# Kernel optimization log

Measured on AMD Instinct MI355X. Metric: run time of the kernel, lower is better.

Reference implementation:

```python
import jax, jax.numpy as jnp
import numpy as np

SCALE_DIM = 64  # output_size, used as 1/sqrt(d) scale per source code


def setup_inputs() -> dict:
    key = jax.random.key(0)
    ks = jax.random.split(key, 6)
    B, S, D_IN, D_OUT = 4, 4096, 512, 64
    return {
        "key_inputs": jax.random.normal(ks[0], (B, S, D_IN), dtype=jnp.float32),
        "value_inputs": jax.random.normal(ks[1], (B, S, D_IN), dtype=jnp.float32),
        "query_inputs": jax.random.normal(ks[2], (B, S, D_IN), dtype=jnp.float32),
        "Wq": jax.random.normal(ks[3], (D_IN, D_OUT), dtype=jnp.float32) * 0.05,
        "Wk": jax.random.normal(ks[4], (D_IN, D_OUT), dtype=jnp.float32) * 0.05,
        "Wv": jax.random.normal(ks[5], (D_IN, D_OUT), dtype=jnp.float32) * 0.05,
    }


def reference(key_inputs, value_inputs, query_inputs, Wq, Wk, Wv):
    # QKV projections: [B,S,D_in] x [D_in,D_out] -> [B,S,D_out]
    Q = jnp.einsum("bsd,de->bse", query_inputs, Wq)
    K = jnp.einsum("bsd,de->bse", key_inputs, Wk)
    V = jnp.einsum("bsd,de->bse", value_inputs, Wv)
    d = K.shape[2]
    # scores: [B, Sq, Sk]
    scores = jnp.einsum("bqe,bke->bqk", Q, K) / jnp.sqrt(jnp.float32(d))
    # causal mask: strictly-upper-triangular -inf (source: transpose(tril(-inf, -1)))
    Sq, Sk = Q.shape[1], K.shape[1]
    causal = jnp.tril(jnp.ones((Sq, Sk), dtype=bool))
    scores = jnp.where(causal[None, :, :], scores, -jnp.inf)
    attn = jax.nn.softmax(scores, axis=-1)
    Z = jnp.einsum("bqk,bke->bqe", attn, V)
    return Z
```

## Files before the change

kernel.cpp:

```cpp
#include <hip/hip_runtime.h>
#include <hip/hip_bf16.h>

#define BATCH 4
#define SEQ   4096
#define DIN   512
#define DOUT  64

typedef __attribute__((ext_vector_type(4))) float f32x4;
typedef __attribute__((ext_vector_type(8))) short bf16x8;
typedef __attribute__((ext_vector_type(4))) short bf16x4;

__device__ __forceinline__ f32x4 mfma16(bf16x8 a, bf16x8 b, f32x4 c) {
    return __builtin_amdgcn_mfma_f32_16x16x32_bf16(a, b, c, 0, 0, 0);
}
__device__ __forceinline__ f32x4 mfma16k(bf16x4 a, bf16x4 b, f32x4 c) {
    return __builtin_amdgcn_mfma_f32_16x16x16bf16_1k(a, b, c, 0, 0, 0);
}

__device__ __forceinline__ short f2bf(float f) {
    union { float f; unsigned u; } x; x.f = f;
    unsigned r = x.u + 0x7FFFu + ((x.u >> 16) & 1u);
    return (short)(r >> 16);
}

__device__ __forceinline__ unsigned pack_bf2(float lo, float hi) {
    union { float f; unsigned u; } a, b; a.f = lo; b.f = hi;
    return __builtin_amdgcn_perm(b.u, a.u, 0x07060302u);
}

__device__ __forceinline__ void dma16(const void* g, void* l) {
    __builtin_amdgcn_global_load_lds(
        (const __attribute__((address_space(1))) void*)g,
        (__attribute__((address_space(3))) void*)l, 16, 0, 0);
}

#define QSCALE 0.1803368801111204f

__global__ __launch_bounds__(256) void wconv_kernel(
    const float* __restrict__ Wq, const float* __restrict__ Wk,
    const float* __restrict__ Wv, short* __restrict__ Wt)
{
    const int m = blockIdx.y;
    const float* W = (m == 0) ? Wq : (m == 1) ? Wk : Wv;
    const int idx = blockIdx.x * 256 + threadIdx.x;
    const int k = idx >> 6;
    const int n = idx & 63;
    Wt[m * (DOUT * DIN) + n * DIN + k] = f2bf(W[idx]);
}

__global__ __launch_bounds__(256) void proj_kernel(
    const float* __restrict__ Xq, const float* __restrict__ Xk, const float* __restrict__ Xv,
    const short* __restrict__ Wt,
    short* __restrict__ Qb, short* __restrict__ Kb, short* __restrict__ Vt)
{
    __shared__ __align__(16) char smem[2][24576];

    const int m = blockIdx.y;
    const float* X  = (m == 0) ? Xq : (m == 1) ? Xk : Xv;
    const short* Wm = Wt + m * (DOUT * DIN);

    const int tid  = threadIdx.x;
    const int wv   = tid >> 6;
    const int lane = tid & 63;
    const int quad = lane >> 4;
    const int l16  = lane & 15;
    const long waveRow = (long)blockIdx.x * 64 + wv * 16;

    const float* xg = X  + (waveRow + l16) * DIN + quad * 8;
    const short* wg = Wm + (long)(wv * 16 + l16) * DIN + quad * 8;

    f32x4 acc[4];
    #pragma unroll
    for (int e = 0; e < 4; ++e) acc[e] = (f32x4){0.f, 0.f, 0.f, 0.f};

#define STAGE_PROJ(B) do {                                   \
        char* xb_ = &smem[(B)][0] + wv * 4096;               \
        char* wb_ = &smem[(B)][0] + 16384 + wv * 2048;       \
        dma16(xg,      xb_);                                 \
        dma16(xg + 4,  xb_ + 1024);                          \
        dma16(xg + 32, xb_ + 2048);                          \
        dma16(xg + 36, xb_ + 3072);                          \
        dma16(wg,      wb_);                                 \
        dma16(wg + 32, wb_ + 1024);                          \
    } while (0)

    STAGE_PROJ(0);
    xg += 64; wg += 64;
    __syncthreads();

    for (int kt = 0; kt < 8; ++kt) {
        const int cur = kt & 1;
        if (kt < 7) {
            if (cur) { STAGE_PROJ(0); } else { STAGE_PROJ(1); }
            xg += 64; wg += 64;
        }
        const char* xb = &smem[cur][0] + wv * 4096;
        const char* wb = &smem[cur][0] + 16384;
        #pragma unroll
        for (int c2 = 0; c2 < 2; ++c2) {
            float4 xa = *(const float4*)(xb + c2 * 2048 + lane * 16);
            float4 xc = *(const float4*)(xb + c2 * 2048 + 1024 + lane * 16);
            bf16x8 af;
            af[0] = f2bf(xa.x); af[1] = f2bf(xa.y); af[2] = f2bf(xa.z); af[3] = f2bf(xa.w);
            af[4] = f2bf(xc.x); af[5] = f2bf(xc.y); af[6] = f2bf(xc.z); af[7] = f2bf(xc.w);
            #pragma unroll
            for (int e = 0; e < 4; ++e) {
                bf16x8 bf = *(const bf16x8*)(wb + (e * 2 + c2) * 1024 + lane * 16);
                if (m < 2) acc[e] = mfma16(af, bf, acc[e]);
                else       acc[e] = mfma16(bf, af, acc[e]);
            }
        }
        __syncthreads();
    }
#undef STAGE_PROJ

    if (m < 2) {
        short* O = (m == 0) ? Qb : Kb;
        const float sc = (m == 0) ? QSCALE : 1.0f;
        #pragma unroll
        for (int e = 0; e < 4; ++e)
            #pragma unroll
            for (int r = 0; r < 4; ++r)
                O[(waveRow + quad * 4 + r) * DOUT + e * 16 + l16] = f2bf(acc[e][r] * sc);
    } else {
        const long b = waveRow >> 12;
        const long s = waveRow & (SEQ - 1);
        #pragma unroll
        for (int e = 0; e < 4; ++e)
            #pragma unroll
            for (int r = 0; r < 4; ++r)
                Vt[(b * DOUT + e * 16 + quad * 4 + r) * SEQ + s + l16] = f2bf(acc[e][r]);
    }
}

__global__ __launch_bounds__(512, 4) void flash_kernel(
    const short* __restrict__ Qb, const short* __restrict__ Kb,
    const short* __restrict__ Vt, float* __restrict__ Out)
{
    __shared__ __align__(16) char smem[2][32768];

    const int i    = blockIdx.x;
    const int b    = (i & 7) >> 1;
    const int half = i >> 8;
    const int v    = (((i >> 3) & 31) << 1) | (i & 1);
    const int t    = half ? v : (127 - v);

    const int tid  = threadIdx.x;
    const int wv   = tid >> 6;
    const int lane = tid & 63;
    const int quad = lane >> 4;
    const int l16  = lane & 15;
    const int wq   = wv >> 2;
    const int wk   = wv & 3;
    const int q0w  = t * 32 + wq * 16;

    const short* Qp = Qb + ((long)b * SEQ + q0w + l16) * DOUT + quad * 8;
    bf16x8 qf0 = *(const bf16x8*)(Qp);
    bf16x8 qf1 = *(const bf16x8*)(Qp + 32);

    const short* Kbase  = Kb + (long)b * SEQ * DOUT;
    const short* VbaseG = Vt + (long)b * DOUT * SEQ;

    const short* gk = Kbase + (long)(wv * 16 + l16) * DOUT + quad * 8;
    const int erow = 4 * wv + quad;
    const int cgr  = l16 ^ (erow & 15);
    const short* gv = VbaseG + (long)erow * SEQ + cgr * 8;

    f32x4 acc[4];
    #pragma unroll
    for (int e = 0; e < 4; ++e) acc[e] = (f32x4){0.f, 0.f, 0.f, 0.f};
    float mrow = -1e30f, lrow = 0.f;

    const int q_hi   = q0w + 15;
    const int qg     = q0w + l16;
    const int wfirst = wk * 32;
    const int R      = t / 4 + 1;

#define STAGE_KV(B, KV0) do {                                         \
        char* kb_ = &smem[(B)][0];                                    \
        char* vb_ = &smem[(B)][0] + 16384;                            \
        const short* gkp_ = gk + (long)(KV0) * DOUT;                  \
        dma16(gkp_,      kb_ + (2 * wv) * 1024);                      \
        dma16(gkp_ + 32, kb_ + (2 * wv + 1) * 1024);                  \
        const short* gvp_ = gv + (KV0);                               \
        dma16(gvp_,            vb_ + (wv)     * 1024);                \
        dma16(gvp_ + 32 * SEQ, vb_ + (wv + 8) * 1024);                \
    } while (0)

    STAGE_KV(0, 0);
    __syncthreads();

    for (int r = 0; r < R; ++r) {
        const int kv0 = r * 128;
        const int cur = r & 1;
        if (r + 1 < R) STAGE_KV(cur ^ 1, kv0 + 128);

        if ((kv0 + wfirst) <= q_hi) {
            const char* kb = &smem[cur][0];
            const char* vb = &smem[cur][0] + 16384;

            f32x4 sc[2];
            #pragma unroll
            for (int kh = 0; kh < 2; ++kh) {
                const int slot = (wk * 2 + kh) * 2;
                bf16x8 k0 = *(const bf16x8*)(kb + slot * 1024 + lane * 16);
                bf16x8 k1 = *(const bf16x8*)(kb + (slot + 1) * 1024 + lane * 16);
                f32x4 z = (f32x4){0.f, 0.f, 0.f, 0.f};
                z = mfma16(k0, qf0, z);
                z = mfma16(k1, qf1, z);
                sc[kh] = z;
            }

            if (kv0 + wfirst + 31 > q0w) {
                #pragma unroll
                for (int kh = 0; kh < 2; ++kh)
                    #pragma unroll
                    for (int rr = 0; rr < 4; ++rr)
                        sc[kh][rr] = ((kv0 + wfirst + kh * 16 + quad * 4 + rr) <= qg)
                                   ? sc[kh][rr] : -1e30f;
            }

            float tm = fmaxf(fmaxf(fmaxf(sc[0][0], sc[0][1]), fmaxf(sc[0][2], sc[0][3])),
                             fmaxf(fmaxf(sc[1][0], sc[1][1]), fmaxf(sc[1][2], sc[1][3])));
            tm = fmaxf(tm, __shfl_xor(tm, 16, 64));
            tm = fmaxf(tm, __shfl_xor(tm, 32, 64));
            if (!__all(tm <= mrow)) {
                const float mn = fmaxf(mrow, tm);
                const float alpha = __builtin_amdgcn_exp2f(mrow - mn);
                mrow = mn;
                lrow *= alpha;
                #pragma unroll
                for (int e = 0; e < 4; ++e)
                    #pragma unroll
                    for (int rr = 0; rr < 4; ++rr) acc[e][rr] *= alpha;
            }
            float p[2][4];
            float rs0 = 0.f, rs1 = 0.f;
            #pragma unroll
            for (int kh = 0; kh < 2; ++kh)
                #pragma unroll
                for (int rr = 0; rr < 4; ++rr) {
                    p[kh][rr] = __builtin_amdgcn_exp2f(sc[kh][rr] - mrow);
                    if (kh == 0) rs0 += p[kh][rr]; else rs1 += p[kh][rr];
                }
            float rs = rs0 + rs1;
            rs += __shfl_xor(rs, 16, 64);
            rs += __shfl_xor(rs, 32, 64);
            lrow += rs;

            union { unsigned u[2]; bf16x4 v; } pf[2];
            #pragma unroll
            for (int kh = 0; kh < 2; ++kh) {
                pf[kh].u[0] = pack_bf2(p[kh][0], p[kh][1]);
                pf[kh].u[1] = pack_bf2(p[kh][2], p[kh][3]);
            }

            #pragma unroll
            for (int kh = 0; kh < 2; ++kh) {
                const int gbase = wk * 4 + kh * 2 + (quad >> 1);
                #pragma unroll
                for (int et = 0; et < 4; ++et) {
                    const int e = et * 16 + l16;
                    bf16x4 cv = *(const bf16x4*)(vb + e * 256
                                   + ((gbase ^ (e & 15)) * 16) + (quad & 1) * 8);
                    acc[et] = mfma16k(cv, pf[kh].v, acc[et]);
                }
            }
        }
        __syncthreads();
    }
#undef STAGE_KV

    float* s_m   = (float*)&smem[0][0];
    float* s_l   = s_m + 128;
    float* s_acc = s_l + 128;

    if (quad == 0) { s_m[wv * 16 + l16] = mrow; s_l[wv * 16 + l16] = lrow; }
    #pragma unroll
    for (int et = 0; et < 4; ++et)
        #pragma unroll
        for (int rr = 0; rr < 4; ++rr)
            s_acc[(wv * 16 + l16) * 65 + et * 16 + quad * 4 + rr] = acc[et][rr];
    __syncthreads();

    const int col   = tid & 63;
    const int rbase = (tid >> 6) * 4;
    float* outp = Out + ((long)b * SEQ + t * 32) * DOUT;
    #pragma unroll
    for (int k = 0; k < 4; ++k) {
        const int row = rbase + k;
        const int w0  = (row >> 4) * 4;
        const int lr  = row & 15;
        const float m0 = s_m[(w0 + 0) * 16 + lr];
        const float m1 = s_m[(w0 + 1) * 16 + lr];
        const float m2 = s_m[(w0 + 2) * 16 + lr];
        const float m3 = s_m[(w0 + 3) * 16 + lr];
        const float mM = fmaxf(fmaxf(m0, m1), fmaxf(m2, m3));
        const float a0 = __builtin_amdgcn_exp2f(m0 - mM);
        const float a1 = __builtin_amdgcn_exp2f(m1 - mM);
        const float a2 = __builtin_amdgcn_exp2f(m2 - mM);
        const float a3 = __builtin_amdgcn_exp2f(m3 - mM);
        const float li = a0 * s_l[(w0 + 0) * 16 + lr] + a1 * s_l[(w0 + 1) * 16 + lr]
                       + a2 * s_l[(w0 + 2) * 16 + lr] + a3 * s_l[(w0 + 3) * 16 + lr];
        const float o  = a0 * s_acc[((w0 + 0) * 16 + lr) * 65 + col]
                       + a1 * s_acc[((w0 + 1) * 16 + lr) * 65 + col]
                       + a2 * s_acc[((w0 + 2) * 16 + lr) * 65 + col]
                       + a3 * s_acc[((w0 + 3) * 16 + lr) * 65 + col];
        outp[row * DOUT + col] = o / li;
    }
}

extern "C" void kernel_launch(void* const* d_in, const int* in_sizes, int n_in,
                              void* d_out, int out_size, void* d_ws, size_t ws_size,
                              hipStream_t stream) {
    const float* key_in   = (const float*)d_in[0];
    const float* value_in = (const float*)d_in[1];
    const float* query_in = (const float*)d_in[2];
    const float* Wq = (const float*)d_in[3];
    const float* Wk = (const float*)d_in[4];
    const float* Wv = (const float*)d_in[5];
    float* out = (float*)d_out;

    short* Qb = (short*)d_ws;
    short* Kb = Qb + (long)BATCH * SEQ * DOUT;
    short* Vt = Kb + (long)BATCH * SEQ * DOUT;
    short* Wt = Vt + (long)BATCH * SEQ * DOUT;

    dim3 wgrid((DOUT * DIN) / 256, 3);
    wconv_kernel<<<wgrid, 256, 0, stream>>>(Wq, Wk, Wv, Wt);

    dim3 pgrid(BATCH * SEQ / 64, 3);
    proj_kernel<<<pgrid, 256, 0, stream>>>(query_in, key_in, value_in,
                                           Wt, Qb, Kb, Vt);

    flash_kernel<<<dim3(SEQ / 32 * BATCH), 512, 0, stream>>>(Qb, Kb, Vt, out);
}
```

Before: 170.3 us.

## Load projection operands directly from global memory instead of LDS double-buffering

The projection kernel drops its shared-memory double-buffered DMA staging and barriers. Each wave now reads its X rows and W columns straight from global memory into registers, unrolled by two, with a launch-bounds occupancy hint of 4. This removes LDS traffic and __syncthreads stalls. In exchange the four waves each re-read the shared W tile from global memory or cache, and latency hiding now depends on occupancy rather than explicit prefetch.

```diff
diff --git a/kernel.cpp b/kernel.cpp
--- a/kernel.cpp
+++ b/kernel.cpp
@@ -48,13 +48,11 @@
     Wt[m * (DOUT * DIN) + n * DIN + k] = f2bf(W[idx]);
 }
 
-__global__ __launch_bounds__(256) void proj_kernel(
+__global__ __launch_bounds__(256, 4) void proj_kernel(
     const float* __restrict__ Xq, const float* __restrict__ Xk, const float* __restrict__ Xv,
     const short* __restrict__ Wt,
     short* __restrict__ Qb, short* __restrict__ Kb, short* __restrict__ Vt)
 {
-    __shared__ __align__(16) char smem[2][24576];
-
     const int m = blockIdx.y;
     const float* X  = (m == 0) ? Xq : (m == 1) ? Xk : Xv;
     const short* Wm = Wt + m * (DOUT * DIN);
@@ -67,52 +65,31 @@
     const long waveRow = (long)blockIdx.x * 64 + wv * 16;
 
     const float* xg = X  + (waveRow + l16) * DIN + quad * 8;
-    const short* wg = Wm + (long)(wv * 16 + l16) * DIN + quad * 8;
+    const short* wg = Wm + (long)l16 * DIN + quad * 8;
 
     f32x4 acc[4];
     #pragma unroll
     for (int e = 0; e < 4; ++e) acc[e] = (f32x4){0.f, 0.f, 0.f, 0.f};
 
-#define STAGE_PROJ(B) do {                                   \
-        char* xb_ = &smem[(B)][0] + wv * 4096;               \
-        char* wb_ = &smem[(B)][0] + 16384 + wv * 2048;       \
-        dma16(xg,      xb_);                                 \
-        dma16(xg + 4,  xb_ + 1024);                          \
-        dma16(xg + 32, xb_ + 2048);                          \
-        dma16(xg + 36, xb_ + 3072);                          \
-        dma16(wg,      wb_);                                 \
-        dma16(wg + 32, wb_ + 1024);                          \
-    } while (0)
-
-    STAGE_PROJ(0);
-    xg += 64; wg += 64;
-    __syncthreads();
-
+    #pragma unroll 2
     for (int kt = 0; kt < 8; ++kt) {
-        const int cur = kt & 1;
-        if (kt < 7) {
-            if (cur) { STAGE_PROJ(0); } else { STAGE_PROJ(1); }
-            xg += 64; wg += 64;
-        }
-        const char* xb = &smem[cur][0] + wv * 4096;
-        const char* wb = &smem[cur][0] + 16384;
+        const float* xk = xg + kt * 64;
+        const short* wk = wg + kt * 64;
         #pragma unroll
         for (int c2 = 0; c2 < 2; ++c2) {
-            float4 xa = *(const float4*)(xb + c2 * 2048 + lane * 16);
-            float4 xc = *(const float4*)(xb + c2 * 2048 + 1024 + lane * 16);
+            float4 xa = *(const float4*)(xk + c2 * 32);
+            float4 xc = *(const float4*)(xk + c2 * 32 + 4);
             bf16x8 af;
             af[0] = f2bf(xa.x); af[1] = f2bf(xa.y); af[2] = f2bf(xa.z); af[3] = f2bf(xa.w);
             af[4] = f2bf(xc.x); af[5] = f2bf(xc.y); af[6] = f2bf(xc.z); af[7] = f2bf(xc.w);
             #pragma unroll
             for (int e = 0; e < 4; ++e) {
-                bf16x8 bf = *(const bf16x8*)(wb + (e * 2 + c2) * 1024 + lane * 16);
+                bf16x8 bf = *(const bf16x8*)(wk + (long)e * 16 * DIN + c2 * 32);
                 if (m < 2) acc[e] = mfma16(af, bf, acc[e]);
                 else       acc[e] = mfma16(bf, af, acc[e]);
             }
         }
-        __syncthreads();
     }
-#undef STAGE_PROJ
 
     if (m < 2) {
         short* O = (m == 0) ? Qb : Kb;
```

Result: slower. 180.6 us (+6.0%).
